# Kernel tuning notes

Hardware: AMD Instinct MI355X
Metric: run time of the kernel (lower is better)

Reference implementation:

```python
import jax, jax.numpy as jnp
import numpy as np

N = 100000   # nodes
E = 1000000  # edges
D = 64       # in_features
D_OUT = 64   # out_features


def setup_inputs() -> dict:
    key = jax.random.key(0)
    k1, k2, k3, k4, k5, k6 = jax.random.split(key, 6)
    h = jax.random.normal(k1, (N, D), dtype=jnp.float32)          # current node features ndata['h']
    i = jax.random.normal(k2, (N, D), dtype=jnp.float32)          # initial features ndata['i']
    edge_src = jax.random.randint(k3, (E,), 0, N, dtype=jnp.int32)
    edge_dst = jax.random.randint(k4, (E,), 0, N, dtype=jnp.int32)
    edge_w = jax.random.uniform(k5, (E,), dtype=jnp.float32)      # scalar edge weight edata['x']
    stdv = 1.0 / np.sqrt(D_OUT)
    weight = jax.random.uniform(k6, (2 * D, D_OUT), dtype=jnp.float32,
                                minval=-stdv, maxval=stdv)        # variant=True -> in = 2*D
    return {
        "h": h, "i": i, "weight": weight, "edge_w": edge_w,
        "lamda": jnp.float32(0.5), "alpha": jnp.float32(0.1),
        "edge_src": edge_src, "edge_dst": edge_dst, "layer_idx": 4,
    }


def reference(h, i, weight, edge_w, lamda, alpha, edge_src, edge_dst, layer_idx):
    # theta = min(1, log(lamda/layer_idx + 1))
    theta = jnp.minimum(jnp.float32(1.0), jnp.log(lamda / layer_idx + 1.0))
    # update_all(u_mul_e('h','x','m'), sum('m','h')): edge-weighted gather-scatter SpMM
    m = h[edge_src] * edge_w[:, None]                 # [E, D]
    h_agg = jax.ops.segment_sum(m, edge_dst, num_segments=h.shape[0])  # [N, D]
    # variant=True branch
    support = jnp.concatenate([h_agg, i], axis=1)     # [N, 2D]
    r = (1.0 - alpha) * h_agg + alpha * i             # [N, D]
    out = theta * (support @ weight) + (1.0 - theta) * r
    # residual=True
    out = out + i
    return out
```

## Files before the change

### kernel.cpp

```cpp
#include <hip/hip_runtime.h>
#include <hip/hip_fp16.h>
#include <math.h>


#define DFEAT 64
#define BINSZ 128
#define NBINS 1024
#define CAP   2048
#define GPAD  16
#define CHUNK 8192
#define BTPB  1024
#define EPT   8
#define SPB   1024

#define ASTR  72

typedef unsigned long long u64;
typedef __attribute__((ext_vector_type(8))) _Float16 f16x8;
typedef __attribute__((ext_vector_type(4))) float f32x4;

__device__ inline unsigned h2u(__half2 h) {
    union { __half2 h; unsigned u; } c; c.h = h; return c.u;
}
__device__ inline __half2 u2h(unsigned u) {
    union { unsigned u; __half2 h; } c; c.u = u; return c.h;
}

__global__ __launch_bounds__(256) void convert_kernel(
    const float* __restrict__ h, const float* __restrict__ weight,
    ushort* __restrict__ h16, ushort* __restrict__ w16,
    int* __restrict__ gcur, int total4) {
    int gid = blockIdx.x * 256 + threadIdx.x;
    int nth = gridDim.x * 256;
    if (gid < NBINS * GPAD) gcur[gid] = 0;
    for (int i = gid; i < total4; i += nth) {
        float4 v = ((const float4*)h)[i];
        uint2 o;
        o.x = h2u(__floats2half2_rn(v.x, v.y));
        o.y = h2u(__floats2half2_rn(v.z, v.w));
        ((uint2*)h16)[i] = o;
    }
    if (gid < 8192) {
        int j = gid & 7, l = (gid >> 3) & 63, cs = gid >> 9;
        int c = cs >> 2, s = cs & 3, q = l >> 4, m = l & 15;
        w16[gid] = __half_as_ushort(
            __float2half_rn(weight[(s * 32 + q * 8 + j) * DFEAT + c * 16 + m]));
    }
}

__global__ __launch_bounds__(1024) void bin_fill_kernel(
    const int* __restrict__ e_src, const int* __restrict__ e_dst,
    const float* __restrict__ e_w, int* __restrict__ gcur,
    u64* __restrict__ bucket, int E) {
    __shared__ u64 staging[CHUNK];
    __shared__ int hist[NBINS];
    __shared__ ushort offs[NBINS];
    __shared__ ushort gbase[NBINS];
    __shared__ int wtot[16];

    int tid = threadIdx.x;
    int e0 = blockIdx.x * CHUNK;
    int cc = min(CHUNK, E - e0);

    hist[tid] = 0;
    __syncthreads();

    int bn[EPT], r[EPT];
    u64 pk[EPT];
#pragma unroll
    for (int j = 0; j < EPT; ++j) {
        int e = e0 + j * BTPB + tid;
        bn[j] = -1;
        if (e < E) {
            int d = e_dst[e];
            int src = e_src[e];
            ushort wb = __half_as_ushort(__float2half_rn(e_w[e]));
            bn[j] = d >> 7;
            pk[j] = ((u64)wb << 48) | ((u64)(unsigned)bn[j] << 33) |
                    ((u64)(unsigned)(d & 127) << 24) | (u64)(unsigned)src;
        }
    }
#pragma unroll
    for (int j = 0; j < EPT; ++j)
        if (bn[j] >= 0) r[j] = atomicAdd(&hist[bn[j]], 1);
    __syncthreads();

    int lane = tid & 63, wv = tid >> 6;
    int c = hist[tid];
    int s = c;
#pragma unroll
    for (int ofs = 1; ofs < 64; ofs <<= 1) {
        int t = __shfl_up(s, ofs);
        if (lane >= ofs) s += t;
    }
    if (lane == 63) wtot[wv] = s;
    __syncthreads();
    int wex = 0;
    if (tid < 64) {
        int v = (tid < 16) ? wtot[tid] : 0;
        int sw = v;
#pragma unroll
        for (int ofs = 1; ofs < 16; ofs <<= 1) {
            int t = __shfl_up(sw, ofs);
            if (tid >= ofs) sw += t;
        }
        if (tid < 16) ((int*)wtot)[tid] = sw - v;
    }
    __syncthreads();
    wex = wtot[wv];
    int excl = wex + (s - c);
    offs[tid] = (ushort)excl;
    __syncthreads();

    {
        int g = c ? atomicAdd(&gcur[tid * GPAD], c) : 0;
        gbase[tid] = (ushort)min(g, CAP);
    }
#pragma unroll
    for (int j = 0; j < EPT; ++j)
        if (bn[j] >= 0) staging[(int)offs[bn[j]] + r[j]] = pk[j];
    __syncthreads();

#pragma unroll
    for (int j = 0; j < EPT; ++j) {
        int p = j * BTPB + tid;
        if (p < cc) {
            u64 e = staging[p];
            int bin = (int)((e >> 33) & 1023);
            int pos = (int)gbase[bin] + (p - (int)offs[bin]);
            if (pos < CAP) {
                bucket[(size_t)bin * CAP + pos] =
                    ((e >> 48) << 32) | (e & 0x7FFFFFFFull);
            }
        }
    }
}

__global__ __launch_bounds__(1024) void spmm_kernel(
    const ushort* __restrict__ h16, const u64* __restrict__ bucket,
    const int* __restrict__ gcur, const ushort* __restrict__ w16,
    const float* __restrict__ ifeat,
    const float* __restrict__ lamda_p, const float* __restrict__ alpha_p,
    const int* __restrict__ layer_p,
    float* __restrict__ out, int N) {
    __shared__ u64 sorted[CAP];
    __shared__ __align__(16) ushort agg16[BINSZ * ASTR];
    __shared__ int hist[BINSZ], start[BINSZ];
    __shared__ int wsum[2];

    int tid = threadIdx.x;
    int bin = blockIdx.x;
    int base = bin << 7;
    int cnt = min(gcur[bin << 4], CAP);
    const u64* bk = bucket + (size_t)bin * CAP;

    if (tid < BINSZ) hist[tid] = 0;
    __syncthreads();

    u64 ev0 = 0, ev1 = 0;
    int dl0 = -1, dl1 = -1, r0 = 0, r1 = 0;
    if (tid < cnt) { ev0 = bk[tid]; dl0 = (int)((ev0 >> 24) & 127); }
    if (tid + SPB < cnt) { ev1 = bk[tid + SPB]; dl1 = (int)((ev1 >> 24) & 127); }
    if (dl0 >= 0) r0 = atomicAdd(&hist[dl0], 1);
    if (dl1 >= 0) r1 = atomicAdd(&hist[dl1], 1);
    __syncthreads();

    int lane = tid & 63, wv = tid >> 6;

    int sv = 0, vv = 0;
    if (tid < 128) {
        vv = hist[tid];
        sv = vv;
#pragma unroll
        for (int ofs = 1; ofs < 64; ofs <<= 1) {
            int t = __shfl_up(sv, ofs);
            if (lane >= ofs) sv += t;
        }
        if (lane == 63) wsum[tid >> 6] = sv;
    }
    __syncthreads();
    if (tid < 128) start[tid] = sv - vv + ((tid >= 64) ? wsum[0] : 0);
    __syncthreads();

    if (dl0 >= 0) sorted[start[dl0] + r0] = ev0;
    if (dl1 >= 0) sorted[start[dl1] + r1] = ev1;
    if (cnt == 0 && tid == 0) sorted[0] = 0;
    __syncthreads();

    int g8 = lane >> 3;
    int m8 = lane & 7;
    int hf = g8 >> 2;
    int gs = g8 & 3;

    int m = lane & 15, q = lane >> 4;
    int t = wv >> 1, ch = wv & 1;
    f16x8 faI[2];
    {
        const float* ip = ifeat + (size_t)min(base + t * 16 + m, N - 1) * DFEAT;
#pragma unroll
        for (int s = 0; s < 2; ++s) {
            float4 v0 = *(const float4*)(ip + s * 32 + q * 8);
            float4 v1 = *(const float4*)(ip + s * 32 + q * 8 + 4);
            f16x8 tt;
            tt[0] = (_Float16)v0.x; tt[1] = (_Float16)v0.y;
            tt[2] = (_Float16)v0.z; tt[3] = (_Float16)v0.w;
            tt[4] = (_Float16)v1.x; tt[5] = (_Float16)v1.y;
            tt[6] = (_Float16)v1.z; tt[7] = (_Float16)v1.w;
            faI[s] = tt;
        }
    }

    for (int kp = 0; kp < 4; ++kp) {
        int nl = (wv << 3) + (kp << 1) + hf;
        int d = hist[nl];
        int b0 = start[nl];
        int hi = (d > 0) ? (b0 + d - 1) : 0;
        __half2 a0 = u2h(0u), a1 = u2h(0u), a2 = u2h(0u), a3 = u2h(0u);
        for (int t0 = 0; t0 < d; t0 += 16) {
#pragma unroll
            for (int s = 0; s < 4; ++s) {
                int idx = t0 + (s << 2) + gs;
                u64 e = sorted[min(b0 + idx, hi)];
                ushort wb = (idx < d) ? (ushort)(e >> 32) : (ushort)0;
                __half2 w2 = __half2half2(__ushort_as_half(wb));
                unsigned src = ((unsigned)e) & 0x1FFFFu;
                uint4 hv = *(const uint4*)(h16 + ((size_t)src << 6) + (m8 << 3));
                a0 = __hfma2(w2, u2h(hv.x), a0);
                a1 = __hfma2(w2, u2h(hv.y), a1);
                a2 = __hfma2(w2, u2h(hv.z), a2);
                a3 = __hfma2(w2, u2h(hv.w), a3);
            }
        }
        a0 = __hadd2(a0, u2h((unsigned)__shfl_xor((int)h2u(a0), 8)));
        a1 = __hadd2(a1, u2h((unsigned)__shfl_xor((int)h2u(a1), 8)));
        a2 = __hadd2(a2, u2h((unsigned)__shfl_xor((int)h2u(a2), 8)));
        a3 = __hadd2(a3, u2h((unsigned)__shfl_xor((int)h2u(a3), 8)));
        a0 = __hadd2(a0, u2h((unsigned)__shfl_xor((int)h2u(a0), 16)));
        a1 = __hadd2(a1, u2h((unsigned)__shfl_xor((int)h2u(a1), 16)));
        a2 = __hadd2(a2, u2h((unsigned)__shfl_xor((int)h2u(a2), 16)));
        a3 = __hadd2(a3, u2h((unsigned)__shfl_xor((int)h2u(a3), 16)));
        if (gs == 0) {
            uint4 o;
            o.x = h2u(a0); o.y = h2u(a1); o.z = h2u(a2); o.w = h2u(a3);
            *(uint4*)(agg16 + nl * ASTR + (m8 << 3)) = o;
        }
    }
    __syncthreads();

    float alf = alpha_p[0];
    float theta = fminf(1.0f, logf(lamda_p[0] / (float)layer_p[0] + 1.0f));

    f16x8 faA[2];
#pragma unroll
    for (int s = 0; s < 2; ++s)
        faA[s] = *(const f16x8*)(agg16 + (t * 16 + m) * ASTR + s * 32 + q * 8);

    f32x4 acc[2] = {{0.f, 0.f, 0.f, 0.f}, {0.f, 0.f, 0.f, 0.f}};
#pragma unroll
    for (int ci = 0; ci < 2; ++ci) {
        int c = ch * 2 + ci;
#pragma unroll
        for (int s = 0; s < 2; ++s) {
            f16x8 bA = *(const f16x8*)(w16 + ((c * 4 + s) * 64 + lane) * 8);
            acc[ci] = __builtin_amdgcn_mfma_f32_16x16x32_f16(faA[s], bA, acc[ci], 0, 0, 0);
            f16x8 bI = *(const f16x8*)(w16 + ((c * 4 + s + 2) * 64 + lane) * 8);
            acc[ci] = __builtin_amdgcn_mfma_f32_16x16x32_f16(faI[s], bI, acc[ci], 0, 0, 0);
        }
    }

#pragma unroll
    for (int ci = 0; ci < 2; ++ci) {
        int c = ch * 2 + ci;
        int col = c * 16 + m;
#pragma unroll
        for (int r = 0; r < 4; ++r) {
            int rowL = t * 16 + q * 4 + r;
            int row = base + rowL;
            if (row < N) {
                float av = __half2float(
                    *(const __half*)(agg16 + rowL * ASTR + col));
                float iv = ifeat[(size_t)row * DFEAT + col];
                out[(size_t)row * DFEAT + col] =
                    theta * acc[ci][r] +
                    (1.f - theta) * ((1.f - alf) * av + alf * iv) + iv;
            }
        }
    }
}

extern "C" void kernel_launch(void* const* d_in, const int* in_sizes, int n_in,
                              void* d_out, int out_size, void* d_ws, size_t ws_size,
                              hipStream_t stream) {
    const float* h       = (const float*)d_in[0];
    const float* ifeat   = (const float*)d_in[1];
    const float* weight  = (const float*)d_in[2];
    const float* edge_w  = (const float*)d_in[3];
    const float* lamda_p = (const float*)d_in[4];
    const float* alpha_p = (const float*)d_in[5];
    const int*   e_src   = (const int*)d_in[6];
    const int*   e_dst   = (const int*)d_in[7];
    const int*   layer_p = (const int*)d_in[8];
    float* out = (float*)d_out;

    int N = in_sizes[0] / DFEAT;
    int E = in_sizes[3];
    int nbins = (N + BINSZ - 1) >> 7;

    int* gcur = (int*)d_ws;
    u64* bucket = (u64*)((char*)d_ws + (size_t)NBINS * GPAD * sizeof(int));
    ushort* h16 = (ushort*)((char*)bucket + (size_t)NBINS * CAP * sizeof(u64));
    ushort* w16 = h16 + (size_t)N * DFEAT;

    int total4 = N * DFEAT / 4;
    convert_kernel<<<2048, 256, 0, stream>>>(h, weight, h16, w16, gcur, total4);

    bin_fill_kernel<<<(E + CHUNK - 1) / CHUNK, BTPB, 0, stream>>>(
        e_src, e_dst, edge_w, gcur, bucket, E);

    spmm_kernel<<<nbins, SPB, 0, stream>>>(
        h16, bucket, gcur, w16, ifeat, lamda_p, alpha_p, layer_p, out, N);
}
```

Baseline: 156.0 us.

## Make SpMM kernel persistent and prefetch next bin's bucket into LDS asynchronously

The SpMM kernel now runs on a grid capped at 512 blocks, and each block loops over bins in strides of 512. While a block gathers and runs MFMA on its current bin, it loads the next bin's edge bucket straight into LDS with global_load_lds DMA. This hides the bucket load latency behind compute. The cost is an extra 16KB of LDS per block, which may lower occupancy, and an uneven split of 782 bins over 512 blocks. Correctness relies on the async LDS writes being waited on before the raw buffer is read.

New measurement: 163.5 us. 4.8% more time.

```diff
diff --git a/kernel.cpp b/kernel.cpp
--- a/kernel.cpp
+++ b/kernel.cpp
@@ -12,6 +12,7 @@
 #define BTPB  1024
 #define EPT   8
 #define SPB   1024
+#define SGRID 512
 
 #define ASTR  72
 
@@ -95,7 +96,6 @@
     }
     if (lane == 63) wtot[wv] = s;
     __syncthreads();
-    int wex = 0;
     if (tid < 64) {
         int v = (tid < 16) ? wtot[tid] : 0;
         int sw = v;
@@ -107,8 +107,7 @@
         if (tid < 16) ((int*)wtot)[tid] = sw - v;
     }
     __syncthreads();
-    wex = wtot[wv];
-    int excl = wex + (s - c);
+    int excl = wtot[wv] + (s - c);
     offs[tid] = (ushort)excl;
     __syncthreads();
 
@@ -136,155 +135,185 @@
     }
 }
 
+__device__ inline void dma_bucket(const u64* bk, void* rawbase, int tid) {
+    const char* g = (const char*)bk + (size_t)tid * 16;
+    char* l = (char*)rawbase + ((tid >> 6) << 10);
+    __builtin_amdgcn_global_load_lds(
+        (const __attribute__((address_space(1))) void*)g,
+        (__attribute__((address_space(3))) void*)l, 16, 0, 0);
+}
+
 __global__ __launch_bounds__(1024) void spmm_kernel(
     const ushort* __restrict__ h16, const u64* __restrict__ bucket,
     const int* __restrict__ gcur, const ushort* __restrict__ w16,
     const float* __restrict__ ifeat,
     const float* __restrict__ lamda_p, const float* __restrict__ alpha_p,
     const int* __restrict__ layer_p,
-    float* __restrict__ out, int N) {
+    float* __restrict__ out, int nbins, int N) {
+    __shared__ __align__(16) u64 raw[CAP];
     __shared__ u64 sorted[CAP];
     __shared__ __align__(16) ushort agg16[BINSZ * ASTR];
     __shared__ int hist[BINSZ], start[BINSZ];
     __shared__ int wsum[2];
 
     int tid = threadIdx.x;
-    int bin = blockIdx.x;
-    int base = bin << 7;
-    int cnt = min(gcur[bin << 4], CAP);
-    const u64* bk = bucket + (size_t)bin * CAP;
-
-    if (tid < BINSZ) hist[tid] = 0;
-    __syncthreads();
-
-    u64 ev0 = 0, ev1 = 0;
-    int dl0 = -1, dl1 = -1, r0 = 0, r1 = 0;
-    if (tid < cnt) { ev0 = bk[tid]; dl0 = (int)((ev0 >> 24) & 127); }
-    if (tid + SPB < cnt) { ev1 = bk[tid + SPB]; dl1 = (int)((ev1 >> 24) & 127); }
-    if (dl0 >= 0) r0 = atomicAdd(&hist[dl0], 1);
-    if (dl1 >= 0) r1 = atomicAdd(&hist[dl1], 1);
-    __syncthreads();
-
     int lane = tid & 63, wv = tid >> 6;
-
-    int sv = 0, vv = 0;
-    if (tid < 128) {
-        vv = hist[tid];
-        sv = vv;
-#pragma unroll
-        for (int ofs = 1; ofs < 64; ofs <<= 1) {
-            int t = __shfl_up(sv, ofs);
-            if (lane >= ofs) sv += t;
-        }
-        if (lane == 63) wsum[tid >> 6] = sv;
-    }
-    __syncthreads();
-    if (tid < 128) start[tid] = sv - vv + ((tid >= 64) ? wsum[0] : 0);
-    __syncthreads();
-
-    if (dl0 >= 0) sorted[start[dl0] + r0] = ev0;
-    if (dl1 >= 0) sorted[start[dl1] + r1] = ev1;
-    if (cnt == 0 && tid == 0) sorted[0] = 0;
-    __syncthreads();
-
     int g8 = lane >> 3;
     int m8 = lane & 7;
     int hf = g8 >> 2;
     int gs = g8 & 3;
-
     int m = lane & 15, q = lane >> 4;
     int t = wv >> 1, ch = wv & 1;
-    f16x8 faI[2];
-    {
-        const float* ip = ifeat + (size_t)min(base + t * 16 + m, N - 1) * DFEAT;
-#pragma unroll
-        for (int s = 0; s < 2; ++s) {
-            float4 v0 = *(const float4*)(ip + s * 32 + q * 8);
-            float4 v1 = *(const float4*)(ip + s * 32 + q * 8 + 4);
-            f16x8 tt;
-            tt[0] = (_Float16)v0.x; tt[1] = (_Float16)v0.y;
-            tt[2] = (_Float16)v0.z; tt[3] = (_Float16)v0.w;
-            tt[4] = (_Float16)v1.x; tt[5] = (_Float16)v1.y;
-            tt[6] = (_Float16)v1.z; tt[7] = (_Float16)v1.w;
-            faI[s] = tt;
-        }
-    }
-
-    for (int kp = 0; kp < 4; ++kp) {
-        int nl = (wv << 3) + (kp << 1) + hf;
-        int d = hist[nl];
-        int b0 = start[nl];
-        int hi = (d > 0) ? (b0 + d - 1) : 0;
-        __half2 a0 = u2h(0u), a1 = u2h(0u), a2 = u2h(0u), a3 = u2h(0u);
-        for (int t0 = 0; t0 < d; t0 += 16) {
-#pragma unroll
-            for (int s = 0; s < 4; ++s) {
-                int idx = t0 + (s << 2) + gs;
-                u64 e = sorted[min(b0 + idx, hi)];
-                ushort wb = (idx < d) ? (ushort)(e >> 32) : (ushort)0;
-                __half2 w2 = __half2half2(__ushort_as_half(wb));
-                unsigned src = ((unsigned)e) & 0x1FFFFu;
-                uint4 hv = *(const uint4*)(h16 + ((size_t)src << 6) + (m8 << 3));
-                a0 = __hfma2(w2, u2h(hv.x), a0);
-                a1 = __hfma2(w2, u2h(hv.y), a1);
-                a2 = __hfma2(w2, u2h(hv.z), a2);
-                a3 = __hfma2(w2, u2h(hv.w), a3);
-            }
-        }
-        a0 = __hadd2(a0, u2h((unsigned)__shfl_xor((int)h2u(a0), 8)));
-        a1 = __hadd2(a1, u2h((unsigned)__shfl_xor((int)h2u(a1), 8)));
-        a2 = __hadd2(a2, u2h((unsigned)__shfl_xor((int)h2u(a2), 8)));
-        a3 = __hadd2(a3, u2h((unsigned)__shfl_xor((int)h2u(a3), 8)));
-        a0 = __hadd2(a0, u2h((unsigned)__shfl_xor((int)h2u(a0), 16)));
-        a1 = __hadd2(a1, u2h((unsigned)__shfl_xor((int)h2u(a1), 16)));
-        a2 = __hadd2(a2, u2h((unsigned)__shfl_xor((int)h2u(a2), 16)));
-        a3 = __hadd2(a3, u2h((unsigned)__shfl_xor((int)h2u(a3), 16)));
-        if (gs == 0) {
-            uint4 o;
-            o.x = h2u(a0); o.y = h2u(a1); o.z = h2u(a2); o.w = h2u(a3);
-            *(uint4*)(agg16 + nl * ASTR + (m8 << 3)) = o;
-        }
-    }
-    __syncthreads();
 
     float alf = alpha_p[0];
     float theta = fminf(1.0f, logf(lamda_p[0] / (float)layer_p[0] + 1.0f));
 
-    f16x8 faA[2];
-#pragma unroll
-    for (int s = 0; s < 2; ++s)
-        faA[s] = *(const f16x8*)(agg16 + (t * 16 + m) * ASTR + s * 32 + q * 8);
-
-    f32x4 acc[2] = {{0.f, 0.f, 0.f, 0.f}, {0.f, 0.f, 0.f, 0.f}};
-#pragma unroll
-    for (int ci = 0; ci < 2; ++ci) {
-        int c = ch * 2 + ci;
-#pragma unroll
-        for (int s = 0; s < 2; ++s) {
-            f16x8 bA = *(const f16x8*)(w16 + ((c * 4 + s) * 64 + lane) * 8);
-            acc[ci] = __builtin_amdgcn_mfma_f32_16x16x32_f16(faA[s], bA, acc[ci], 0, 0, 0);
-            f16x8 bI = *(const f16x8*)(w16 + ((c * 4 + s + 2) * 64 + lane) * 8);
-            acc[ci] = __builtin_amdgcn_mfma_f32_16x16x32_f16(faI[s], bI, acc[ci], 0, 0, 0);
-        }
-    }
-
-#pragma unroll
-    for (int ci = 0; ci < 2; ++ci) {
-        int c = ch * 2 + ci;
-        int col = c * 16 + m;
-#pragma unroll
-        for (int r = 0; r < 4; ++r) {
-            int rowL = t * 16 + q * 4 + r;
-            int row = base + rowL;
-            if (row < N) {
-                float av = __half2float(
-                    *(const __half*)(agg16 + rowL * ASTR + col));
-                float iv = ifeat[(size_t)row * DFEAT + col];
-                out[(size_t)row * DFEAT + col] =
-                    theta * acc[ci][r] +
-                    (1.f - theta) * ((1.f - alf) * av + alf * iv) + iv;
-            }
-        }
+    int bin = blockIdx.x;
+    if (bin >= nbins) return;
+    int cnt = min(gcur[bin << 4], CAP);
+    dma_bucket(bucket + (size_t)bin * CAP, raw, tid);
+
+    for (;;) {
+        int base = bin << 7;
+
+        if (tid < BINSZ) hist[tid] = 0;
+        __syncthreads();
+
+        u64 ev0 = raw[tid];
+        u64 ev1 = raw[tid + SPB];
+        int dl0 = (tid < cnt) ? (int)((ev0 >> 24) & 127) : -1;
+        int dl1 = (tid + SPB < cnt) ? (int)((ev1 >> 24) & 127) : -1;
+        int r0 = 0, r1 = 0;
+        if (dl0 >= 0) r0 = atomicAdd(&hist[dl0], 1);
+        if (dl1 >= 0) r1 = atomicAdd(&hist[dl1], 1);
+        __syncthreads();
+
+        int sv = 0, vv = 0;
+        if (tid < 128) {
+            vv = hist[tid];
+            sv = vv;
+#pragma unroll
+            for (int ofs = 1; ofs < 64; ofs <<= 1) {
+                int tt = __shfl_up(sv, ofs);
+                if (lane >= ofs) sv += tt;
+            }
+            if (lane == 63) wsum[tid >> 6] = sv;
+        }
+        __syncthreads();
+        if (tid < 128) start[tid] = sv - vv + ((tid >= 64) ? wsum[0] : 0);
+        __syncthreads();
+
+        if (dl0 >= 0) sorted[start[dl0] + r0] = ev0;
+        if (dl1 >= 0) sorted[start[dl1] + r1] = ev1;
+        if (cnt == 0 && tid == 0) sorted[0] = 0;
+        __syncthreads();
+
+        int nbin = bin + SGRID;
+        int ncnt = 0;
+        if (nbin < nbins) {
+            ncnt = min(gcur[nbin << 4], CAP);
+            dma_bucket(bucket + (size_t)nbin * CAP, raw, tid);
+        }
+
+        f16x8 faI[2];
+        {
+            const float* ip =
+                ifeat + (size_t)min(base + t * 16 + m, N - 1) * DFEAT;
+#pragma unroll
+            for (int s = 0; s < 2; ++s) {
+                float4 v0 = *(const float4*)(ip + s * 32 + q * 8);
+                float4 v1 = *(const float4*)(ip + s * 32 + q * 8 + 4);
+                f16x8 tt;
+                tt[0] = (_Float16)v0.x; tt[1] = (_Float16)v0.y;
+                tt[2] = (_Float16)v0.z; tt[3] = (_Float16)v0.w;
+                tt[4] = (_Float16)v1.x; tt[5] = (_Float16)v1.y;
+                tt[6] = (_Float16)v1.z; tt[7] = (_Float16)v1.w;
+                faI[s] = tt;
+            }
+        }
+
+        for (int kp = 0; kp < 4; ++kp) {
+            int nl = (wv << 3) + (kp << 1) + hf;
+            int d = hist[nl];
+            int b0 = start[nl];
+            int hi = (d > 0) ? (b0 + d - 1) : 0;
+            __half2 a0 = u2h(0u), a1 = u2h(0u), a2 = u2h(0u), a3 = u2h(0u);
+            for (int t0 = 0; t0 < d; t0 += 16) {
+#pragma unroll
+                for (int s = 0; s < 4; ++s) {
+                    int idx = t0 + (s << 2) + gs;
+                    u64 e = sorted[min(b0 + idx, hi)];
+                    ushort wb = (idx < d) ? (ushort)(e >> 32) : (ushort)0;
+                    __half2 w2 = __half2half2(__ushort_as_half(wb));
+                    unsigned src = ((unsigned)e) & 0x1FFFFu;
+                    uint4 hv =
+                        *(const uint4*)(h16 + ((size_t)src << 6) + (m8 << 3));
+                    a0 = __hfma2(w2, u2h(hv.x), a0);
+                    a1 = __hfma2(w2, u2h(hv.y), a1);
+                    a2 = __hfma2(w2, u2h(hv.z), a2);
+                    a3 = __hfma2(w2, u2h(hv.w), a3);
+                }
+            }
+            a0 = __hadd2(a0, u2h((unsigned)__shfl_xor((int)h2u(a0), 8)));
+            a1 = __hadd2(a1, u2h((unsigned)__shfl_xor((int)h2u(a1), 8)));
+            a2 = __hadd2(a2, u2h((unsigned)__shfl_xor((int)h2u(a2), 8)));
+            a3 = __hadd2(a3, u2h((unsigned)__shfl_xor((int)h2u(a3), 8)));
+            a0 = __hadd2(a0, u2h((unsigned)__shfl_xor((int)h2u(a0), 16)));
+            a1 = __hadd2(a1, u2h((unsigned)__shfl_xor((int)h2u(a1), 16)));
+            a2 = __hadd2(a2, u2h((unsigned)__shfl_xor((int)h2u(a2), 16)));
+            a3 = __hadd2(a3, u2h((unsigned)__shfl_xor((int)h2u(a3), 16)));
+            if (gs == 0) {
+                uint4 o;
+                o.x = h2u(a0); o.y = h2u(a1); o.z = h2u(a2); o.w = h2u(a3);
+                *(uint4*)(agg16 + nl * ASTR + (m8 << 3)) = o;
+            }
+        }
+        __syncthreads();
+
+        f16x8 faA[2];
+#pragma unroll
+        for (int s = 0; s < 2; ++s)
+            faA[s] =
+                *(const f16x8*)(agg16 + (t * 16 + m) * ASTR + s * 32 + q * 8);
+
+        f32x4 acc[2] = {{0.f, 0.f, 0.f, 0.f}, {0.f, 0.f, 0.f, 0.f}};
+#pragma unroll
+        for (int ci = 0; ci < 2; ++ci) {
+            int c = ch * 2 + ci;
+#pragma unroll
+            for (int s = 0; s < 2; ++s) {
+                f16x8 bA = *(const f16x8*)(w16 + ((c * 4 + s) * 64 + lane) * 8);
+                acc[ci] = __builtin_amdgcn_mfma_f32_16x16x32_f16(
+                    faA[s], bA, acc[ci], 0, 0, 0);
+                f16x8 bI =
+                    *(const f16x8*)(w16 + ((c * 4 + s + 2) * 64 + lane) * 8);
+                acc[ci] = __builtin_amdgcn_mfma_f32_16x16x32_f16(
+                    faI[s], bI, acc[ci], 0, 0, 0);
+            }
+        }
+
+#pragma unroll
+        for (int ci = 0; ci < 2; ++ci) {
+            int c = ch * 2 + ci;
+            int col = c * 16 + m;
+#pragma unroll
+            for (int r = 0; r < 4; ++r) {
+                int rowL = t * 16 + q * 4 + r;
+                int row = base + rowL;
+                if (row < N) {
+                    float av = __half2float(
+                        *(const __half*)(agg16 + rowL * ASTR + col));
+                    float iv = ifeat[(size_t)row * DFEAT + col];
+                    out[(size_t)row * DFEAT + col] =
+                        theta * acc[ci][r] +
+                        (1.f - theta) * ((1.f - alf) * av + alf * iv) + iv;
+                }
+            }
+        }
+
+        if (nbin >= nbins) break;
+        bin = nbin;
+        cnt = ncnt;
     }
 }
 
@@ -317,6 +346,8 @@
     bin_fill_kernel<<<(E + CHUNK - 1) / CHUNK, BTPB, 0, stream>>>(
         e_src, e_dst, edge_w, gcur, bucket, E);
 
-    spmm_kernel<<<nbins, SPB, 0, stream>>>(
-        h16, bucket, gcur, w16, ifeat, lamda_p, alpha_p, layer_p, out, N);
-}
+    int sgrid = nbins < SGRID ? nbins : SGRID;
+    spmm_kernel<<<sgrid, SPB, 0, stream>>>(
+        h16, bucket, gcur, w16, ifeat, lamda_p, alpha_p, layer_p, out,
+        nbins, N);
+}
```
